# Performance work log

Hardware: AMD Instinct MI355X
Metric: run time of the kernel (lower is better)

## Reference

```python
import jax, jax.numpy as jnp
import numpy as np

D, N, K = 6, 32768, 16          # depths, nodes per depth, max children
V, DIN, DOUT = 100000, 64, 64   # vocab, embed dim, hidden dim


def setup_inputs() -> dict:
    key = jax.random.key(0)
    ks = jax.random.split(key, 6)
    labels = jax.random.randint(ks[0], (D, N), 0, V, dtype=jnp.int32)
    # child index 0 == no child (masked); 1..N index previous depth's nodes
    child_idx = jax.random.randint(ks[1], (D, N, K), 0, N + 1, dtype=jnp.int32)
    E = jax.random.uniform(ks[2], (V, DIN), jnp.float32, -0.05, 0.05)
    s_in = 1.0 / np.sqrt(DIN)
    W_w = jax.random.uniform(ks[3], (DIN, 4 * DOUT), jnp.float32, -s_in, s_in)
    W_b = jnp.zeros((4 * DOUT,), jnp.float32)
    s_out = 1.0 / np.sqrt(DOUT)
    U_f = jax.random.uniform(ks[4], (DOUT, DOUT), jnp.float32, -s_out, s_out)
    U_iuo = jax.random.uniform(ks[5], (DOUT, 3 * DOUT), jnp.float32, -s_out, s_out)
    return {"labels": labels, "child_idx": child_idx, "E": E,
            "W_w": W_w, "W_b": W_b, "U_f": U_f, "U_iuo": U_iuo}


def _tree_lstm(labels, child_idx, E, W_w, W_b, U_f, U_iuo):
    d = U_f.shape[0]
    n = labels.shape[1]
    zero_row = jnp.zeros((1, d), jnp.float32)

    def step(carry, inp):
        h_prev, c_prev = carry            # [N+1, d], row 0 = zero init state
        lab, idx = inp                    # [N], [N, K]
        x = E[lab]                        # [N, din] embedding lookup
        mask = (idx != 0).astype(jnp.float32)   # [N, K]
        h = h_prev[idx]                   # [N, K, d] gather children hidden
        c = c_prev[idx]                   # [N, K, d] gather children cell
        h_sum = jnp.einsum('nkd,nk->nd', h, mask)  # masked child-sum
        Wx = x @ W_w + W_b                # [N, 4d]
        W_f_x, W_i_x, W_u_x, W_o_x = jnp.split(Wx, 4, axis=-1)
        # per-child forget gate
        f_k = jax.nn.sigmoid(W_f_x[:, None, :] + jnp.einsum('nkd,de->nke', h, U_f))
        branch_f = jnp.einsum('nkd,nkd,nk->nd', f_k, c, mask)
        iuo = h_sum @ U_iuo               # [N, 3d]
        i_g = jax.nn.sigmoid(iuo[:, :d] + W_i_x)
        u_g = jnp.tanh(iuo[:, d:2 * d] + W_u_x)
        o_g = jax.nn.sigmoid(iuo[:, 2 * d:] + W_o_x)
        new_c = i_g * u_g + branch_f
        new_h = o_g * jnp.tanh(new_c)
        h_next = jnp.concatenate([zero_row, new_h], 0)
        c_next = jnp.concatenate([zero_row, new_c], 0)
        return (h_next, c_next), None

    init = (jnp.zeros((n + 1, d), jnp.float32), jnp.zeros((n + 1, d), jnp.float32))
    (h_fin, _c_fin), _ = jax.lax.scan(step, init, (labels, child_idx))
    return h_fin[1:]                      # final-depth (roots) hidden [N, d]


def reference(labels, child_idx, E, W_w, W_b, U_f, U_iuo):
    return _tree_lstm(labels, child_idx, E, W_w, W_b, U_f, U_iuo)
```

## Files before the change

kernel.cpp:

```cpp
#include <hip/hip_runtime.h>

#define NN 32768
#define KK 16
#define DD 6

typedef short short8 __attribute__((ext_vector_type(8)));
typedef float floatx4 __attribute__((ext_vector_type(4)));
typedef _Float16 half4v __attribute__((ext_vector_type(4)));
typedef _Float16 half8 __attribute__((ext_vector_type(8)));

__device__ __forceinline__ float sigm(float x) { return 1.0f / (1.0f + __expf(-x)); }
__device__ __forceinline__ float ftanh(float x) {
    float e = __expf(2.0f * x);
    return 1.0f - 2.0f / (e + 1.0f);
}
__device__ __forceinline__ unsigned short f2bf(float x) {
    union { float f; unsigned u; } v; v.f = x;
    unsigned r = v.u + 0x7FFF + ((v.u >> 16) & 1);
    return (unsigned short)(r >> 16);
}
__device__ __forceinline__ float bf2f(unsigned short h) {
    union { unsigned u; float f; } v; v.u = ((unsigned)h) << 16; return v.f;
}

__global__ __launch_bounds__(256) void k_prep(
    const float* __restrict__ W_w, const float* __restrict__ U_iuo,
    const float* __restrict__ U_f,
    unsigned short* __restrict__ WwF, unsigned short* __restrict__ BiF,
    _Float16* __restrict__ BfF)
{
    const int t = blockIdx.x * 256 + threadIdx.x;
    if (t < 16384) {
        const int u = t, j = u & 7, ln = (u >> 3) & 63, ks = (u >> 9) & 1, nt = u >> 10;
        const int col = nt * 16 + (ln & 15), k = ks * 32 + (ln >> 4) * 8 + j;
        WwF[u] = f2bf(W_w[k * 256 + col]);
    } else if (t < 28672) {
        const int u = t - 16384, j = u & 7, ln = (u >> 3) & 63, ks = (u >> 9) & 1, nt = u >> 10;
        const int col = nt * 16 + (ln & 15), k = ks * 32 + (ln >> 4) * 8 + j;
        BiF[u] = f2bf(U_iuo[k * 192 + col]);
    } else {
        const int u = t - 28672, j = u & 7, ln = (u >> 3) & 63, ks = (u >> 9) & 1, nt = u >> 10;
        const int col = nt * 16 + (ln & 15), k = ks * 32 + (ln >> 4) * 8 + j;
        BfF[u] = (_Float16)U_f[k * 64 + col];
    }
}

__global__ __launch_bounds__(256) void k0_all(
    const int* __restrict__ labels, const float* __restrict__ E,
    const unsigned short* __restrict__ WwF, const float* __restrict__ W_b,
    _Float16* __restrict__ WxF)
{
    const int tid = threadIdx.x;
    const int blk = blockIdx.x & 511;
    const int dep = blockIdx.x >> 9;
    const int n0 = blk * 64;
    const int ln = tid & 63, wv = tid >> 6;
    const int lr = ln & 15, qd = ln >> 4;
    const int lab = labels[(size_t)dep * NN + n0 + wv * 16 + lr];
    const float4* __restrict__ e4 = (const float4*)(E + (size_t)lab * 64);
    short8 af[2];
#pragma unroll
    for (int ks = 0; ks < 2; ++ks) {
        const float4 v0 = e4[ks * 8 + qd * 2 + 0];
        const float4 v1 = e4[ks * 8 + qd * 2 + 1];
        short8 a;
        a[0] = (short)f2bf(v0.x); a[1] = (short)f2bf(v0.y);
        a[2] = (short)f2bf(v0.z); a[3] = (short)f2bf(v0.w);
        a[4] = (short)f2bf(v1.x); a[5] = (short)f2bf(v1.y);
        a[6] = (short)f2bf(v1.z); a[7] = (short)f2bf(v1.w);
        af[ks] = a;
    }
    const short8* __restrict__ bw = (const short8*)WwF;
    _Float16* __restrict__ base =
        WxF + ((size_t)(dep * 512 + blk) * 4 + wv) * 16 * 256 + (size_t)ln * 4;
#pragma unroll
    for (int nt = 0; nt < 16; ++nt) {
        floatx4 a = (floatx4){0.f, 0.f, 0.f, 0.f};
        a = __builtin_amdgcn_mfma_f32_16x16x32_bf16(af[0], bw[(nt * 2 + 0) * 64 + ln], a, 0, 0, 0);
        a = __builtin_amdgcn_mfma_f32_16x16x32_bf16(af[1], bw[(nt * 2 + 1) * 64 + ln], a, 0, 0, 0);
        const float bb = W_b[nt * 16 + lr];
        half4v hv;
#pragma unroll
        for (int r = 0; r < 4; ++r) hv[r] = (_Float16)(a[r] + bb);
        *(half4v*)&base[nt * 256] = hv;
    }
}

__global__ __launch_bounds__(256, 4) void kd_fused(
    const int* __restrict__ cidx, const _Float16* __restrict__ sprev,
    const _Float16* __restrict__ Wx, const unsigned short* __restrict__ BiF,
    const _Float16* __restrict__ BfF, _Float16* __restrict__ snext,
    float* __restrict__ out, int first, int last)
{
    __shared__ __align__(16) _Float16 BfL[4096];
    __shared__ __align__(16) unsigned char stage[4 * 4352];
    const int tid = threadIdx.x;
    {
        const half8* __restrict__ src = (const half8*)BfF;
        half8* dst = (half8*)BfL;
        dst[tid] = src[tid];
        dst[tid + 256] = src[tid + 256];
    }
    const int ln = tid & 63, wv = tid >> 6;
    const int g = wv & 1, kh = wv >> 1;
    const int lr = ln & 15, qd = ln >> 4;
    const int n0 = blockIdx.x * 32;
    unsigned char* const myst = stage + wv * 4352;
    const _Float16* __restrict__ wbase =
        Wx + ((size_t)(blockIdx.x >> 1) * 4 + (blockIdx.x & 1) * 2 + g) * 4096 + (size_t)ln * 4;
    __syncthreads();

    float hsA[2][8];
    float bfv[4][4];
#pragma unroll
    for (int ks = 0; ks < 2; ++ks)
#pragma unroll
        for (int j = 0; j < 8; ++j) hsA[ks][j] = 0.f;
#pragma unroll
    for (int r = 0; r < 4; ++r)
#pragma unroll
        for (int nt = 0; nt < 4; ++nt) bfv[r][nt] = 0.f;

    if (!first) {
        float wfx[4][4];
#pragma unroll
        for (int nt = 0; nt < 4; ++nt) {
            const half4v fv = *(const half4v*)&wbase[nt * 256];
#pragma unroll
            for (int r = 0; r < 4; ++r) wfx[r][nt] = (float)fv[r];
        }
        const int m = ln >> 2, ch = ln & 3;
        const size_t ib = (size_t)(n0 + g * 16 + m) * KK + kh * 8;
        const uint4* __restrict__ sp4 = (const uint4*)sprev;
        uint4* const st4 = (uint4*)myst;
        const half8* __restrict__ bl = (const half8*)BfL;
        {
            const int id = cidx[ib];
            uint4 rb[4];
#pragma unroll
            for (int i = 0; i < 4; ++i) rb[i] = sp4[(size_t)id * 16 + ch + 4 * i];
#pragma unroll
            for (int i = 0; i < 4; ++i) st4[m * 17 + ch + 4 * i] = rb[i];
        }
#pragma unroll 1
        for (int kk = 0; kk < 8; ++kk) {
            uint4 nb[4];
            if (kk < 7) {
                const int idn = cidx[ib + kk + 1];
#pragma unroll
                for (int i = 0; i < 4; ++i) nb[i] = sp4[(size_t)idn * 16 + ch + 4 * i];
            }
            const half8 hf0 = *(const half8*)(myst + lr * 272 + qd * 16);
            const half8 hf1 = *(const half8*)(myst + lr * 272 + 64 + qd * 16);
            half4v cq[4];
#pragma unroll
            for (int r = 0; r < 4; ++r)
                cq[r] = *(const half4v*)(myst + (qd * 4 + r) * 272 + 128 + lr * 8);
#pragma unroll
            for (int nt = 0; nt < 4; ++nt) {
                floatx4 gg = (floatx4){0.f, 0.f, 0.f, 0.f};
                gg = __builtin_amdgcn_mfma_f32_16x16x32_f16(hf0, bl[(nt * 2 + 0) * 64 + ln], gg, 0, 0, 0);
                gg = __builtin_amdgcn_mfma_f32_16x16x32_f16(hf1, bl[(nt * 2 + 1) * 64 + ln], gg, 0, 0, 0);
#pragma unroll
                for (int r = 0; r < 4; ++r)
                    bfv[r][nt] = fmaf(sigm(wfx[r][nt] + gg[r]), (float)cq[r][nt], bfv[r][nt]);
            }
#pragma unroll
            for (int j = 0; j < 8; ++j) {
                hsA[0][j] += (float)hf0[j];
                hsA[1][j] += (float)hf1[j];
            }
            if (kk < 7) {
#pragma unroll
                for (int i = 0; i < 4; ++i) st4[m * 17 + ch + 4 * i] = nb[i];
            }
        }
        __syncthreads();
        float* const pbh = (float*)(stage + g * 4352);
        float* const pbb = (float*)(stage + (2 + g) * 4352);
        if (kh == 1) {
#pragma unroll
            for (int ks = 0; ks < 2; ++ks)
#pragma unroll
                for (int j = 0; j < 8; ++j) pbh[ln * 17 + ks * 8 + j] = hsA[ks][j];
#pragma unroll
            for (int r = 0; r < 4; ++r)
#pragma unroll
                for (int nt = 0; nt < 4; ++nt) pbb[ln * 17 + r * 4 + nt] = bfv[r][nt];
        }
        __syncthreads();
        if (kh == 0) {
#pragma unroll
            for (int ks = 0; ks < 2; ++ks)
#pragma unroll
                for (int j = 0; j < 8; ++j) hsA[ks][j] += pbh[ln * 17 + ks * 8 + j];
#pragma unroll
            for (int r = 0; r < 4; ++r)
#pragma unroll
                for (int nt = 0; nt < 4; ++nt) bfv[r][nt] += pbb[ln * 17 + r * 4 + nt];
        }
    }
    if (kh == 0) {
        floatx4 acc[12];
#pragma unroll
        for (int nt = 0; nt < 12; ++nt) acc[nt] = (floatx4){0.f, 0.f, 0.f, 0.f};
        if (!first) {
            short8 ahi[2], alo[2];
#pragma unroll
            for (int ks = 0; ks < 2; ++ks)
#pragma unroll
                for (int j = 0; j < 8; ++j) {
                    const float v = hsA[ks][j];
                    const unsigned short hi = f2bf(v);
                    ahi[ks][j] = (short)hi;
                    alo[ks][j] = (short)f2bf(v - bf2f(hi));
                }
            const short8* __restrict__ bi = (const short8*)BiF;
#pragma unroll
            for (int nt = 0; nt < 12; ++nt) {
                floatx4 a = (floatx4){0.f, 0.f, 0.f, 0.f};
#pragma unroll
                for (int ks = 0; ks < 2; ++ks) {
                    const short8 bu = bi[(nt * 2 + ks) * 64 + ln];
                    a = __builtin_amdgcn_mfma_f32_16x16x32_bf16(alo[ks], bu, a, 0, 0, 0);
                    a = __builtin_amdgcn_mfma_f32_16x16x32_bf16(ahi[ks], bu, a, 0, 0, 0);
                }
                acc[nt] = a;
            }
        }
        _Float16* const rb = (_Float16*)myst;
#pragma unroll
        for (int nt = 0; nt < 4; ++nt) {
            const half4v iv = *(const half4v*)&wbase[(4 + nt) * 256];
            const half4v uv = *(const half4v*)&wbase[(8 + nt) * 256];
            const half4v ov = *(const half4v*)&wbase[(12 + nt) * 256];
#pragma unroll
            for (int r = 0; r < 4; ++r) {
                const int mrow = qd * 4 + r;
                const float ig = sigm(acc[nt][r] + (float)iv[r]);
                const float ug = ftanh(acc[4 + nt][r] + (float)uv[r]);
                const float og = sigm(acc[8 + nt][r] + (float)ov[r]);
                const float nc = fmaf(ig, ug, bfv[r][nt]);
                const float nh = og * ftanh(nc);
                if (last) {
                    out[(size_t)(n0 + g * 16 + mrow) * 64 + nt * 16 + lr] = nh;
                } else {
                    rb[mrow * 128 + nt * 16 + lr] = (_Float16)nh;
                    rb[mrow * 128 + 64 + lr * 4 + nt] = (_Float16)nc;
                }
            }
        }
        if (!last) {
            const uint4* const s4 = (const uint4*)myst;
            uint4* const d4 = (uint4*)((char*)snext + (size_t)(n0 + g * 16 + 1) * 256);
#pragma unroll
            for (int i = 0; i < 4; ++i) d4[ln + i * 64] = s4[ln + i * 64];
        }
    }
    if (!last && blockIdx.x == 0 && tid < 64)
        ((unsigned*)snext)[tid] = 0u;
}

extern "C" void kernel_launch(void* const* d_in, const int* in_sizes, int n_in,
                              void* d_out, int out_size, void* d_ws, size_t ws_size,
                              hipStream_t stream)
{
    const int*   labels = (const int*)d_in[0];
    const int*   child  = (const int*)d_in[1];
    const float* E      = (const float*)d_in[2];
    const float* W_w    = (const float*)d_in[3];
    const float* W_b    = (const float*)d_in[4];
    const float* U_f    = (const float*)d_in[5];
    const float* U_iuo  = (const float*)d_in[6];
    float* out = (float*)d_out;

    _Float16* s0 = (_Float16*)d_ws;
    _Float16* s1 = s0 + (size_t)(NN + 1) * 128;
    _Float16* WxF = s1 + (size_t)(NN + 1) * 128;
    unsigned short* WwF = (unsigned short*)(WxF + (size_t)6 * NN * 256);
    unsigned short* BiF = WwF + 16384;
    _Float16* BfF = (_Float16*)(BiF + 12288);

    k_prep<<<128, 256, 0, stream>>>(W_w, U_iuo, U_f, WwF, BiF, BfF);
    k0_all<<<6 * (NN / 64), 256, 0, stream>>>(labels, E, WwF, W_b, WxF);

    _Float16* sp = s0;
    _Float16* sn = s1;
    for (int d = 0; d < DD; ++d) {
        const int last = (d == DD - 1);
        kd_fused<<<NN / 32, 256, 0, stream>>>(
            child + (size_t)d * NN * KK, sp,
            WxF + (size_t)d * NN * 256,
            BiF, BfF, sn, out, d == 0, last);
        _Float16* ts = sp; sp = sn; sn = ts;
    }
}
```

Baseline: 405.9 us.

## Fuse input projection into per-depth kernel and double-buffer child gathers

The separate k0_all kernel that precomputed the x·W_w+b projection for all depths into a large fp16 workspace is removed. Each per-depth kernel now performs the embedding lookup and computes the projection with MFMA inline: the forget-gate part up front and the i/u/o parts at the epilogue. This avoids writing and re-reading the projection buffer through HBM. The child gather loop is also fully unrolled with two register buffers, and the child indices are loaded as vectors, to overlap gathers with compute. In exchange the kernel does redundant per-node MFMA work in the critical path, uses more registers (launch bounds lowered to 3 blocks per CU), and the projection is now kept in fp32 rather than rounded to fp16.

```diff
diff --git a/kernel.cpp b/kernel.cpp
--- a/kernel.cpp
+++ b/kernel.cpp
@@ -45,18 +45,29 @@
     }
 }
 
-__global__ __launch_bounds__(256) void k0_all(
-    const int* __restrict__ labels, const float* __restrict__ E,
+__global__ __launch_bounds__(256, 3) void kd_fused(
+    const int* __restrict__ cidx, const int* __restrict__ labels,
+    const float* __restrict__ E, const _Float16* __restrict__ sprev,
     const unsigned short* __restrict__ WwF, const float* __restrict__ W_b,
-    _Float16* __restrict__ WxF)
+    const unsigned short* __restrict__ BiF, const _Float16* __restrict__ BfF,
+    _Float16* __restrict__ snext, float* __restrict__ out, int first, int last)
 {
+    __shared__ __align__(16) _Float16 BfL[4096];
+    __shared__ __align__(16) unsigned char stage[4 * 4352];
     const int tid = threadIdx.x;
-    const int blk = blockIdx.x & 511;
-    const int dep = blockIdx.x >> 9;
-    const int n0 = blk * 64;
+    {
+        const half8* __restrict__ src = (const half8*)BfF;
+        half8* dst = (half8*)BfL;
+        dst[tid] = src[tid];
+        dst[tid + 256] = src[tid + 256];
+    }
     const int ln = tid & 63, wv = tid >> 6;
+    const int g = wv & 1, kh = wv >> 1;
     const int lr = ln & 15, qd = ln >> 4;
-    const int lab = labels[(size_t)dep * NN + n0 + wv * 16 + lr];
+    const int n0 = blockIdx.x * 32;
+    unsigned char* const myst = stage + wv * 4352;
+
+    const int lab = labels[n0 + g * 16 + lr];
     const float4* __restrict__ e4 = (const float4*)(E + (size_t)lab * 64);
     short8 af[2];
 #pragma unroll
@@ -71,43 +82,16 @@
         af[ks] = a;
     }
     const short8* __restrict__ bw = (const short8*)WwF;
-    _Float16* __restrict__ base =
-        WxF + ((size_t)(dep * 512 + blk) * 4 + wv) * 16 * 256 + (size_t)ln * 4;
-#pragma unroll
-    for (int nt = 0; nt < 16; ++nt) {
+    float wfx[4][4];
+#pragma unroll
+    for (int nt = 0; nt < 4; ++nt) {
         floatx4 a = (floatx4){0.f, 0.f, 0.f, 0.f};
         a = __builtin_amdgcn_mfma_f32_16x16x32_bf16(af[0], bw[(nt * 2 + 0) * 64 + ln], a, 0, 0, 0);
         a = __builtin_amdgcn_mfma_f32_16x16x32_bf16(af[1], bw[(nt * 2 + 1) * 64 + ln], a, 0, 0, 0);
         const float bb = W_b[nt * 16 + lr];
-        half4v hv;
-#pragma unroll
-        for (int r = 0; r < 4; ++r) hv[r] = (_Float16)(a[r] + bb);
-        *(half4v*)&base[nt * 256] = hv;
-    }
-}
-
-__global__ __launch_bounds__(256, 4) void kd_fused(
-    const int* __restrict__ cidx, const _Float16* __restrict__ sprev,
-    const _Float16* __restrict__ Wx, const unsigned short* __restrict__ BiF,
-    const _Float16* __restrict__ BfF, _Float16* __restrict__ snext,
-    float* __restrict__ out, int first, int last)
-{
-    __shared__ __align__(16) _Float16 BfL[4096];
-    __shared__ __align__(16) unsigned char stage[4 * 4352];
-    const int tid = threadIdx.x;
-    {
-        const half8* __restrict__ src = (const half8*)BfF;
-        half8* dst = (half8*)BfL;
-        dst[tid] = src[tid];
-        dst[tid + 256] = src[tid + 256];
-    }
-    const int ln = tid & 63, wv = tid >> 6;
-    const int g = wv & 1, kh = wv >> 1;
-    const int lr = ln & 15, qd = ln >> 4;
-    const int n0 = blockIdx.x * 32;
-    unsigned char* const myst = stage + wv * 4352;
-    const _Float16* __restrict__ wbase =
-        Wx + ((size_t)(blockIdx.x >> 1) * 4 + (blockIdx.x & 1) * 2 + g) * 4096 + (size_t)ln * 4;
+#pragma unroll
+        for (int r = 0; r < 4; ++r) wfx[r][nt] = a[r] + bb;
+    }
     __syncthreads();
 
     float hsA[2][8];
@@ -122,59 +106,53 @@
         for (int nt = 0; nt < 4; ++nt) bfv[r][nt] = 0.f;
 
     if (!first) {
-        float wfx[4][4];
-#pragma unroll
-        for (int nt = 0; nt < 4; ++nt) {
-            const half4v fv = *(const half4v*)&wbase[nt * 256];
-#pragma unroll
-            for (int r = 0; r < 4; ++r) wfx[r][nt] = (float)fv[r];
-        }
         const int m = ln >> 2, ch = ln & 3;
         const size_t ib = (size_t)(n0 + g * 16 + m) * KK + kh * 8;
         const uint4* __restrict__ sp4 = (const uint4*)sprev;
         uint4* const st4 = (uint4*)myst;
         const half8* __restrict__ bl = (const half8*)BfL;
-        {
-            const int id = cidx[ib];
-            uint4 rb[4];
-#pragma unroll
-            for (int i = 0; i < 4; ++i) rb[i] = sp4[(size_t)id * 16 + ch + 4 * i];
-#pragma unroll
-            for (int i = 0; i < 4; ++i) st4[m * 17 + ch + 4 * i] = rb[i];
-        }
-#pragma unroll 1
-        for (int kk = 0; kk < 8; ++kk) {
-            uint4 nb[4];
-            if (kk < 7) {
-                const int idn = cidx[ib + kk + 1];
-#pragma unroll
-                for (int i = 0; i < 4; ++i) nb[i] = sp4[(size_t)idn * 16 + ch + 4 * i];
-            }
-            const half8 hf0 = *(const half8*)(myst + lr * 272 + qd * 16);
-            const half8 hf1 = *(const half8*)(myst + lr * 272 + 64 + qd * 16);
-            half4v cq[4];
-#pragma unroll
-            for (int r = 0; r < 4; ++r)
-                cq[r] = *(const half4v*)(myst + (qd * 4 + r) * 272 + 128 + lr * 8);
-#pragma unroll
-            for (int nt = 0; nt < 4; ++nt) {
-                floatx4 gg = (floatx4){0.f, 0.f, 0.f, 0.f};
-                gg = __builtin_amdgcn_mfma_f32_16x16x32_f16(hf0, bl[(nt * 2 + 0) * 64 + ln], gg, 0, 0, 0);
-                gg = __builtin_amdgcn_mfma_f32_16x16x32_f16(hf1, bl[(nt * 2 + 1) * 64 + ln], gg, 0, 0, 0);
-#pragma unroll
-                for (int r = 0; r < 4; ++r)
-                    bfv[r][nt] = fmaf(sigm(wfx[r][nt] + gg[r]), (float)cq[r][nt], bfv[r][nt]);
-            }
-#pragma unroll
-            for (int j = 0; j < 8; ++j) {
-                hsA[0][j] += (float)hf0[j];
-                hsA[1][j] += (float)hf1[j];
-            }
-            if (kk < 7) {
-#pragma unroll
-                for (int i = 0; i < 4; ++i) st4[m * 17 + ch + 4 * i] = nb[i];
-            }
-        }
+        const int4 idv0 = *(const int4*)&cidx[ib];
+        const int4 idv1 = *(const int4*)&cidx[ib + 4];
+        uint4 A0, A1, A2, A3, B0, B1, B2, B3;
+
+#define GLOAD(R0, R1, R2, R3, idv) {                                   \
+        const size_t b_ = (size_t)(idv) * 16 + ch;                     \
+        R0 = sp4[b_]; R1 = sp4[b_ + 4]; R2 = sp4[b_ + 8]; R3 = sp4[b_ + 12]; }
+#define SWRITE(R0, R1, R2, R3) {                                       \
+        st4[m * 17 + ch] = R0;      st4[m * 17 + ch + 4] = R1;         \
+        st4[m * 17 + ch + 8] = R2;  st4[m * 17 + ch + 12] = R3; }
+#define BODY() {                                                       \
+        const half8 hf0 = *(const half8*)(myst + lr * 272 + qd * 16);  \
+        const half8 hf1 = *(const half8*)(myst + lr * 272 + 64 + qd * 16); \
+        half4v cq[4];                                                  \
+        _Pragma("unroll") for (int r = 0; r < 4; ++r)                  \
+            cq[r] = *(const half4v*)(myst + (qd * 4 + r) * 272 + 128 + lr * 8); \
+        _Pragma("unroll") for (int nt = 0; nt < 4; ++nt) {             \
+            floatx4 gg = (floatx4){0.f, 0.f, 0.f, 0.f};                \
+            gg = __builtin_amdgcn_mfma_f32_16x16x32_f16(hf0, bl[(nt * 2 + 0) * 64 + ln], gg, 0, 0, 0); \
+            gg = __builtin_amdgcn_mfma_f32_16x16x32_f16(hf1, bl[(nt * 2 + 1) * 64 + ln], gg, 0, 0, 0); \
+            _Pragma("unroll") for (int r = 0; r < 4; ++r)              \
+                bfv[r][nt] = fmaf(sigm(wfx[r][nt] + gg[r]), (float)cq[r][nt], bfv[r][nt]); \
+        }                                                              \
+        _Pragma("unroll") for (int j = 0; j < 8; ++j) {                \
+            hsA[0][j] += (float)hf0[j]; hsA[1][j] += (float)hf1[j]; } }
+
+        GLOAD(A0, A1, A2, A3, idv0.x);
+        GLOAD(B0, B1, B2, B3, idv0.y);
+        SWRITE(A0, A1, A2, A3);
+        GLOAD(A0, A1, A2, A3, idv0.z);
+        BODY(); SWRITE(B0, B1, B2, B3); GLOAD(B0, B1, B2, B3, idv0.w);
+        BODY(); SWRITE(A0, A1, A2, A3); GLOAD(A0, A1, A2, A3, idv1.x);
+        BODY(); SWRITE(B0, B1, B2, B3); GLOAD(B0, B1, B2, B3, idv1.y);
+        BODY(); SWRITE(A0, A1, A2, A3); GLOAD(A0, A1, A2, A3, idv1.z);
+        BODY(); SWRITE(B0, B1, B2, B3); GLOAD(B0, B1, B2, B3, idv1.w);
+        BODY(); SWRITE(A0, A1, A2, A3);
+        BODY(); SWRITE(B0, B1, B2, B3);
+        BODY();
+#undef GLOAD
+#undef SWRITE
+#undef BODY
+
         __syncthreads();
         float* const pbh = (float*)(stage + g * 4352);
         float* const pbb = (float*)(stage + (2 + g) * 4352);
@@ -231,15 +209,24 @@
         _Float16* const rb = (_Float16*)myst;
 #pragma unroll
         for (int nt = 0; nt < 4; ++nt) {
-            const half4v iv = *(const half4v*)&wbase[(4 + nt) * 256];
-            const half4v uv = *(const half4v*)&wbase[(8 + nt) * 256];
-            const half4v ov = *(const half4v*)&wbase[(12 + nt) * 256];
+            floatx4 wi = (floatx4){0.f, 0.f, 0.f, 0.f};
+            floatx4 wu = (floatx4){0.f, 0.f, 0.f, 0.f};
+            floatx4 wo = (floatx4){0.f, 0.f, 0.f, 0.f};
+            wi = __builtin_amdgcn_mfma_f32_16x16x32_bf16(af[0], bw[((4 + nt) * 2 + 0) * 64 + ln], wi, 0, 0, 0);
+            wi = __builtin_amdgcn_mfma_f32_16x16x32_bf16(af[1], bw[((4 + nt) * 2 + 1) * 64 + ln], wi, 0, 0, 0);
+            wu = __builtin_amdgcn_mfma_f32_16x16x32_bf16(af[0], bw[((8 + nt) * 2 + 0) * 64 + ln], wu, 0, 0, 0);
+            wu = __builtin_amdgcn_mfma_f32_16x16x32_bf16(af[1], bw[((8 + nt) * 2 + 1) * 64 + ln], wu, 0, 0, 0);
+            wo = __builtin_amdgcn_mfma_f32_16x16x32_bf16(af[0], bw[((12 + nt) * 2 + 0) * 64 + ln], wo, 0, 0, 0);
+            wo = __builtin_amdgcn_mfma_f32_16x16x32_bf16(af[1], bw[((12 + nt) * 2 + 1) * 64 + ln], wo, 0, 0, 0);
+            const float bi_ = W_b[(4 + nt) * 16 + lr];
+            const float bu_ = W_b[(8 + nt) * 16 + lr];
+            const float bo_ = W_b[(12 + nt) * 16 + lr];
 #pragma unroll
             for (int r = 0; r < 4; ++r) {
                 const int mrow = qd * 4 + r;
-                const float ig = sigm(acc[nt][r] + (float)iv[r]);
-                const float ug = ftanh(acc[4 + nt][r] + (float)uv[r]);
-                const float og = sigm(acc[8 + nt][r] + (float)ov[r]);
+                const float ig = sigm(acc[nt][r] + wi[r] + bi_);
+                const float ug = ftanh(acc[4 + nt][r] + wu[r] + bu_);
+                const float og = sigm(acc[8 + nt][r] + wo[r] + bo_);
                 const float nc = fmaf(ig, ug, bfv[r][nt]);
                 const float nh = og * ftanh(nc);
                 if (last) {
@@ -276,22 +263,19 @@
 
     _Float16* s0 = (_Float16*)d_ws;
     _Float16* s1 = s0 + (size_t)(NN + 1) * 128;
-    _Float16* WxF = s1 + (size_t)(NN + 1) * 128;
-    unsigned short* WwF = (unsigned short*)(WxF + (size_t)6 * NN * 256);
+    unsigned short* WwF = (unsigned short*)(s1 + (size_t)(NN + 1) * 128);
     unsigned short* BiF = WwF + 16384;
     _Float16* BfF = (_Float16*)(BiF + 12288);
 
     k_prep<<<128, 256, 0, stream>>>(W_w, U_iuo, U_f, WwF, BiF, BfF);
-    k0_all<<<6 * (NN / 64), 256, 0, stream>>>(labels, E, WwF, W_b, WxF);
 
     _Float16* sp = s0;
     _Float16* sn = s1;
     for (int d = 0; d < DD; ++d) {
         const int last = (d == DD - 1);
         kd_fused<<<NN / 32, 256, 0, stream>>>(
-            child + (size_t)d * NN * KK, sp,
-            WxF + (size_t)d * NN * 256,
-            BiF, BfF, sn, out, d == 0, last);
+            child + (size_t)d * NN * KK, labels + (size_t)d * NN, E, sp,
+            WwF, W_b, BiF, BfF, sn, out, d == 0, last);
         _Float16* ts = sp; sp = sn; sn = ts;
     }
 }
```

New measurement: 547.6 us. +34.9%, slower.
